# Kernel optimization log

Hardware: AMD Instinct MI355X
Metric: run time of the kernel (lower is better)

Reference implementation:

```python
import jax, jax.numpy as jnp
import numpy as np

N_HEADS = 16
N_KV = 8
HEAD_DIM = 128
HID = 2048
GROUPS = N_HEADS // N_KV
THETA = 10000.0


def _rope_cos_sin(position_ids, dtype):
    # position_ids: [1, S] int
    inv_freq = 1.0 / (THETA ** (jnp.arange(0, HEAD_DIM, 2, dtype=jnp.float32) / HEAD_DIM))
    freqs = position_ids.astype(jnp.float32)[:, :, None] * inv_freq[None, None, :]  # [1,S,hd/2]
    emb = jnp.concatenate([freqs, freqs], axis=-1)  # [1,S,hd]
    return jnp.cos(emb).astype(dtype)[:, None, :, :], jnp.sin(emb).astype(dtype)[:, None, :, :]


def _rotate_half(x):
    x1, x2 = x[..., : HEAD_DIM // 2], x[..., HEAD_DIM // 2 :]
    return jnp.concatenate([-x2, x1], axis=-1)


def setup_inputs() -> dict:
    key = jax.random.key(0)
    ks = jax.random.split(key, 8)
    B, S = 2, 2048
    hidden_states = jax.random.normal(ks[0], (B, S, HID), jnp.float32)
    Wq = jax.random.normal(ks[1], (HID, N_HEADS * HEAD_DIM), jnp.float32) * 0.02
    Wk = jax.random.normal(ks[2], (HID, N_KV * HEAD_DIM), jnp.float32) * 0.02
    Wv = jax.random.normal(ks[3], (HID, N_KV * HEAD_DIM), jnp.float32) * 0.02
    Wo = jax.random.normal(ks[4], (HID, HID), jnp.float32) * 0.02
    gate = jnp.zeros((1, N_HEADS, 1, 1), jnp.float32)
    memory_in = jax.random.normal(ks[5], (B, N_KV, HEAD_DIM, HEAD_DIM), jnp.float32)
    norm_in = jax.random.uniform(ks[6], (B, N_KV, 1, HEAD_DIM), jnp.float32)
    position_ids = jnp.arange(S, dtype=jnp.int32)[None, :]
    return {"hidden_states": hidden_states, "Wq": Wq, "Wk": Wk, "Wv": Wv, "Wo": Wo,
            "gate": gate, "memory_in": memory_in, "norm_in": norm_in,
            "position_ids": position_ids}


def reference(hidden_states, Wq, Wk, Wv, Wo, gate, memory_in, norm_in, position_ids):
    B, S, _ = hidden_states.shape
    # projections -> [B, H, S, hd]
    q = jnp.einsum('bsh,ho->bso', hidden_states, Wq).reshape(B, S, N_HEADS, HEAD_DIM).transpose(0, 2, 1, 3)
    k = jnp.einsum('bsh,ho->bso', hidden_states, Wk).reshape(B, S, N_KV, HEAD_DIM).transpose(0, 2, 1, 3)
    v = jnp.einsum('bsh,ho->bso', hidden_states, Wv).reshape(B, S, N_KV, HEAD_DIM).transpose(0, 2, 1, 3)

    # ---- compressive memory retrieval (pre-RoPE q, as in original) ----
    sigma_q = jax.nn.elu(q) + 1.0  # [B, nH, S, hd]
    mem_tiled = jnp.tile(memory_in, (1, GROUPS, 1, 1))          # torch .repeat tiles
    norm_tiled = jnp.tile(norm_in, (1, GROUPS, 1, 1))            # [B, nH, 1, hd]
    memory_output = jnp.einsum('bhsd,bhde->bhse', sigma_q, mem_tiled)
    norm_bcast = jnp.einsum('bhsd,bhd->bhs', sigma_q, norm_tiled[:, :, 0, :])[..., None]
    memory_output = memory_output / norm_bcast

    # ---- memory update (pre-RoPE k, v) ----
    sigma_k = jax.nn.elu(k) + 1.0  # [B, nKV, S, hd]
    updated_memory = memory_in + jnp.einsum('bhsd,bhse->bhde', sigma_k, v)
    updated_norm = norm_in + jnp.sum(sigma_k, axis=2, keepdims=True)

    # ---- RoPE ----
    cos, sin = _rope_cos_sin(position_ids, q.dtype)
    q = q * cos + _rotate_half(q) * sin
    k = k * cos + _rotate_half(k) * sin

    # ---- repeat_kv (interleave, groups) ----
    k = jnp.repeat(k, GROUPS, axis=1)
    v = jnp.repeat(v, GROUPS, axis=1)

    # ---- causal SDPA ----
    scale = 1.0 / np.sqrt(HEAD_DIM)
    scores = jnp.einsum('bhqd,bhkd->bhqk', q, k) * scale
    causal = jnp.tril(jnp.ones((S, S), dtype=bool))
    scores = jnp.where(causal[None, None], scores, jnp.finfo(scores.dtype).min)
    probs = jax.nn.softmax(scores, axis=-1)
    attn = jnp.einsum('bhqk,bhkd->bhqd', probs, v)

    # ---- gated combination + output projection ----
    g = jax.nn.sigmoid(gate)
    combined = g * memory_output + (1.0 - g) * attn  # [B, nH, S, hd]
    combined = combined.transpose(0, 2, 1, 3).reshape(B, S, HID)
    final_output = jnp.einsum('bsh,ho->bso', combined, Wo)
    return final_output, updated_memory, updated_norm
```

## Files before the change

kernel.cpp:

```cpp
#include <hip/hip_runtime.h>

#define BATCH 2
#define SEQ   2048
#define HID   2048
#define NH    16
#define NKV   8
#define HD    128
#define M_ROWS (BATCH * SEQ)
#define QKV_N  4096

typedef __attribute__((ext_vector_type(8))) __bf16 bf16x8;
typedef __attribute__((ext_vector_type(4))) float  f32x4;

static __device__ __forceinline__ f32x4 mfma16(bf16x8 a, bf16x8 b, f32x4 c) {
    return __builtin_amdgcn_mfma_f32_16x16x32_bf16(a, b, c, 0, 0, 0);
}
static __device__ __forceinline__ float sigma_f(float x) {
    return x > 0.f ? x + 1.f : __expf(x);
}
static __device__ __forceinline__ void gload16(const __bf16* g, __bf16* l) {
    __builtin_amdgcn_global_load_lds(
        (const __attribute__((address_space(1))) void*)g,
        (__attribute__((address_space(3))) void*)l, 16, 0, 0);
}

#define OFF_QKV  0ull
#define OFF_SQ   67108864ull
#define OFF_QR   83886080ull
#define OFF_KR   100663296ull
#define OFF_VT   109051904ull
#define OFF_ND   117440512ull
#define OFF_CB   117702656ull
#define OFF_PART 134479872ull
#define OFF_BND  142868480ull
#define OFF_MAXP 143130624ull
#define OFF_NPART 143134720ull
#define NSPLIT 8

__global__ void f2b_k(const float* __restrict__ src, __bf16* __restrict__ dst)
{
    const size_t i = ((size_t)blockIdx.x * 256 + threadIdx.x) * 8;
    const float4 v0 = *reinterpret_cast<const float4*>(src + i);
    const float4 v1 = *reinterpret_cast<const float4*>(src + i + 4);
    bf16x8 t;
    t[0]=(__bf16)v0.x; t[1]=(__bf16)v0.y; t[2]=(__bf16)v0.z; t[3]=(__bf16)v0.w;
    t[4]=(__bf16)v1.x; t[5]=(__bf16)v1.y; t[6]=(__bf16)v1.z; t[7]=(__bf16)v1.w;
    *reinterpret_cast<bf16x8*>(dst + i) = t;
}

__global__ __launch_bounds__(256) void tr_k(const float* __restrict__ W,
                                            __bf16* __restrict__ Bt, int K, int N)
{
    __shared__ __bf16 T[64][72];
    const int k0 = blockIdx.x * 64, n0 = blockIdx.y * 64;
    const int t = threadIdx.x;
    #pragma unroll
    for (int i = 0; i < 4; ++i) {
        const int idx = t + i * 256;
        const int r = idx >> 4, c4 = (idx & 15) * 4;
        const float4 v = *reinterpret_cast<const float4*>(&W[(size_t)(k0 + r) * N + n0 + c4]);
        T[c4 + 0][r] = (__bf16)v.x; T[c4 + 1][r] = (__bf16)v.y;
        T[c4 + 2][r] = (__bf16)v.z; T[c4 + 3][r] = (__bf16)v.w;
    }
    __syncthreads();
    #pragma unroll
    for (int i = 0; i < 2; ++i) {
        const int idx = t + i * 256;
        const int rr = idx >> 3, cc = (idx & 7) * 8;
        *reinterpret_cast<bf16x8*>(&Bt[(size_t)(n0 + rr) * K + k0 + cc]) =
            *reinterpret_cast<bf16x8*>(&T[rr][cc]);
    }
}

__global__ __launch_bounds__(256) void gemm_bt(const __bf16* __restrict__ A,
                                               const __bf16* __restrict__ Bt,
                                               float* __restrict__ C,
                                               int N, int K)
{
    __shared__ __align__(16) __bf16 As[128 * 32];
    __shared__ __align__(16) __bf16 Bs[128 * 32];

    const int tid = threadIdx.x, wave = tid >> 6, lane = tid & 63;
    const int l15 = lane & 15, l4 = lane >> 4;
    const int m0 = blockIdx.x * 128, n0 = blockIdx.y * 128;
    const int wm = (wave & 1) * 64, wn = (wave >> 1) * 64;

    f32x4 acc[4][4] = {};

    const int srow = wave * 32 + (lane >> 2);
    const int scol = (lane & 3) * 8;
    const __bf16* Ab = A  + (size_t)(m0 + srow) * K + scol;
    const __bf16* Bb = Bt + (size_t)(n0 + srow) * K + scol;
    __bf16* AsB0 = &As[(wave * 32) * 32];
    __bf16* AsB1 = &As[(wave * 32 + 16) * 32];
    __bf16* BsB0 = &Bs[(wave * 32) * 32];
    __bf16* BsB1 = &Bs[(wave * 32 + 16) * 32];

    for (int kb = 0; kb < K; kb += 32) {
        gload16(Ab + kb,            AsB0);
        gload16(Ab + 16 * K + kb,   AsB1);
        gload16(Bb + kb,            BsB0);
        gload16(Bb + 16 * K + kb,   BsB1);
        __syncthreads();

        bf16x8 af[4], bfr[4];
        #pragma unroll
        for (int mt = 0; mt < 4; ++mt)
            af[mt] = *reinterpret_cast<bf16x8*>(&As[(wm + mt * 16 + l15) * 32 + l4 * 8]);
        #pragma unroll
        for (int nt = 0; nt < 4; ++nt)
            bfr[nt] = *reinterpret_cast<bf16x8*>(&Bs[(wn + nt * 16 + l15) * 32 + l4 * 8]);
        #pragma unroll
        for (int mt = 0; mt < 4; ++mt)
            #pragma unroll
            for (int nt = 0; nt < 4; ++nt)
                acc[mt][nt] = mfma16(af[mt], bfr[nt], acc[mt][nt]);
        __syncthreads();
    }

    #pragma unroll
    for (int mt = 0; mt < 4; ++mt)
        #pragma unroll
        for (int nt = 0; nt < 4; ++nt)
            #pragma unroll
            for (int r = 0; r < 4; ++r) {
                const int row = m0 + wm + mt * 16 + l4 * 4 + r;
                const int col = n0 + wn + nt * 16 + l15;
                C[(size_t)row * N + col] = acc[mt][nt][r];
            }
}

__global__ __launch_bounds__(256) void prep_k(const float* __restrict__ qkv,
                                              const float* __restrict__ norm_in,
                                              const int* __restrict__ pos_ids,
                                              __bf16* __restrict__ sq, __bf16* __restrict__ qr,
                                              __bf16* __restrict__ kr, __bf16* __restrict__ vt,
                                              float* __restrict__ nd, float* __restrict__ bnd,
                                              float* __restrict__ maxp)
{
    const int sc = blockIdx.x, kvh = blockIdx.y, b = blockIdx.z;
    const int s0 = sc * 32, t = threadIdx.x;
    const float scale = 0.08838834764831845f;
    const float s2 = scale * scale;
    const float NEG_LN_TH = -0.14391156831212787f;
    __shared__ float krn[32];

    {
        const int row = t >> 2;
        const int head = row >> 5, sl = row & 31;
        const int hq = kvh * 2 + head, nh = hq & 7;
        const int dq = (t & 3) * 16;
        const int pos = pos_ids[s0 + sl];
        const float* qp = qkv + (size_t)(b * SEQ + s0 + sl) * QKV_N + hq * 128;
        const float* np = norm_in + (b * NKV + nh) * 128;

        float x0[16], x1[16];
        #pragma unroll
        for (int i = 0; i < 16; i += 4) {
            *reinterpret_cast<float4*>(&x0[i]) = *reinterpret_cast<const float4*>(qp + dq + i);
            *reinterpret_cast<float4*>(&x1[i]) = *reinterpret_cast<const float4*>(qp + dq + 64 + i);
        }
        float nds = 0.f, qns = 0.f;
        bf16x8 sqv0[2], sqv1[2], qrv0[2], qrv1[2];
        #pragma unroll
        for (int i = 0; i < 16; ++i) {
            const int j = dq + i;
            float c, sn;
            __sincosf((float)pos * __expf((float)j * NEG_LN_TH), &sn, &c);
            qrv0[i >> 3][i & 7] = (__bf16)((x0[i] * c - x1[i] * sn) * scale);
            qrv1[i >> 3][i & 7] = (__bf16)((x1[i] * c + x0[i] * sn) * scale);
            const float sg0 = sigma_f(x0[i]), sg1 = sigma_f(x1[i]);
            sqv0[i >> 3][i & 7] = (__bf16)sg0;
            sqv1[i >> 3][i & 7] = (__bf16)sg1;
            nds += sg0 * np[j] + sg1 * np[j + 64];
            qns += (x0[i] * x0[i] + x1[i] * x1[i]) * s2;
        }
        __bf16* sqp = sq + ((size_t)(b * NH + hq) * SEQ + s0 + sl) * 128;
        __bf16* qrp = qr + ((size_t)(b * NH + hq) * SEQ + s0 + sl) * 128;
        *reinterpret_cast<bf16x8*>(sqp + dq)      = sqv0[0];
        *reinterpret_cast<bf16x8*>(sqp + dq + 8)  = sqv0[1];
        *reinterpret_cast<bf16x8*>(sqp + dq + 64) = sqv1[0];
        *reinterpret_cast<bf16x8*>(sqp + dq + 72) = sqv1[1];
        *reinterpret_cast<bf16x8*>(qrp + dq)      = qrv0[0];
        *reinterpret_cast<bf16x8*>(qrp + dq + 8)  = qrv0[1];
        *reinterpret_cast<bf16x8*>(qrp + dq + 64) = qrv1[0];
        *reinterpret_cast<bf16x8*>(qrp + dq + 72) = qrv1[1];

        nds += __shfl_xor(nds, 1); nds += __shfl_xor(nds, 2);
        qns += __shfl_xor(qns, 1); qns += __shfl_xor(qns, 2);
        if ((t & 3) == 0) {
            nd [(size_t)(b * NH + hq) * SEQ + s0 + sl] = nds;
            bnd[(size_t)(b * NH + hq) * SEQ + s0 + sl] = qns;
        }
    }

    if (t < 128) {
        const int sl = t >> 2;
        const int dq = (t & 3) * 16;
        const int pos = pos_ids[s0 + sl];
        const float* kp = qkv + (size_t)(b * SEQ + s0 + sl) * QKV_N + 2048 + kvh * 128;
        float x0[16], x1[16];
        #pragma unroll
        for (int i = 0; i < 16; i += 4) {
            *reinterpret_cast<float4*>(&x0[i]) = *reinterpret_cast<const float4*>(kp + dq + i);
            *reinterpret_cast<float4*>(&x1[i]) = *reinterpret_cast<const float4*>(kp + dq + 64 + i);
        }
        bf16x8 kv0[2], kv1[2];
        float kns = 0.f;
        #pragma unroll
        for (int i = 0; i < 16; ++i) {
            const int j = dq + i;
            float c, sn;
            __sincosf((float)pos * __expf((float)j * NEG_LN_TH), &sn, &c);
            kv0[i >> 3][i & 7] = (__bf16)(x0[i] * c - x1[i] * sn);
            kv1[i >> 3][i & 7] = (__bf16)(x1[i] * c + x0[i] * sn);
            kns += x0[i] * x0[i] + x1[i] * x1[i];
        }
        __bf16* krp = kr + ((size_t)(b * NKV + kvh) * SEQ + s0 + sl) * 128;
        *reinterpret_cast<bf16x8*>(krp + dq)      = kv0[0];
        *reinterpret_cast<bf16x8*>(krp + dq + 8)  = kv0[1];
        *reinterpret_cast<bf16x8*>(krp + dq + 64) = kv1[0];
        *reinterpret_cast<bf16x8*>(krp + dq + 72) = kv1[1];
        kns += __shfl_xor(kns, 1); kns += __shfl_xor(kns, 2);
        if ((t & 3) == 0) krn[sl] = kns;
    }

    __shared__ float vl[128][33];
    {
        const int sl = t >> 3, dch = (t & 7) * 16;
        const float* vp = qkv + (size_t)(b * SEQ + s0 + sl) * QKV_N + 3072 + kvh * 128 + dch;
        float xv[16];
        #pragma unroll
        for (int i = 0; i < 16; i += 4)
            *reinterpret_cast<float4*>(&xv[i]) = *reinterpret_cast<const float4*>(vp + i);
        #pragma unroll
        for (int i = 0; i < 16; ++i) vl[dch + i][sl] = xv[i];
    }
    __syncthreads();
    if (t == 0) {
        float mx = 0.f;
        #pragma unroll
        for (int i = 0; i < 32; ++i) mx = fmaxf(mx, krn[i]);
        maxp[((b * NKV + kvh) << 6) + sc] = mx;
    }
    {
        const int d = t >> 1, sh = (t & 1) * 16;
        bf16x8 o0, o1;
        #pragma unroll
        for (int j = 0; j < 8; ++j) o0[j] = (__bf16)vl[d][sh + j];
        #pragma unroll
        for (int j = 0; j < 8; ++j) o1[j] = (__bf16)vl[d][sh + 8 + j];
        __bf16* vp = vt + ((size_t)((b * NKV + kvh) * 128 + d)) * SEQ + s0 + sh;
        *reinterpret_cast<bf16x8*>(vp)     = o0;
        *reinterpret_cast<bf16x8*>(vp + 8) = o1;
    }
}

__global__ __launch_bounds__(256) void memout_k(const __bf16* __restrict__ sq,
                                                const float* __restrict__ mem_in,
                                                const float* __restrict__ nd,
                                                const float* __restrict__ gate,
                                                __bf16* __restrict__ cb)
{
    __shared__ __align__(16) __bf16 mt[128][136];
    const int tid = threadIdx.x;
    const int h = blockIdx.y, b = blockIdx.z;
    const int s0 = blockIdx.x * 64;

    const float* mem = mem_in + (size_t)(b * NKV + (h & 7)) * 16384;
    for (int i = tid; i < 16384; i += 256) {
        int dd = i >> 7, e = i & 127;
        mt[e][dd] = (__bf16)mem[i];
    }
    __syncthreads();

    const int wave = tid >> 6, lane = tid & 63, l15 = lane & 15, l4 = lane >> 4;
    f32x4 acc[8] = {};
    const __bf16* sqb = sq + ((size_t)(b * NH + h) * SEQ + s0 + wave * 16 + l15) * 128;
    #pragma unroll
    for (int kb = 0; kb < 4; ++kb) {
        bf16x8 a = *reinterpret_cast<const bf16x8*>(sqb + kb * 32 + l4 * 8);
        #pragma unroll
        for (int nc = 0; nc < 8; ++nc) {
            bf16x8 bb = *reinterpret_cast<bf16x8*>(&mt[nc * 16 + l15][kb * 32 + l4 * 8]);
            acc[nc] = mfma16(a, bb, acc[nc]);
        }
    }
    float g = 1.f / (1.f + __expf(-gate[h]));
    #pragma unroll
    for (int r = 0; r < 4; ++r) {
        int srow = s0 + wave * 16 + l4 * 4 + r;
        float scl = g / nd[(size_t)(b * NH + h) * SEQ + srow];
        __bf16* cbp = cb + (size_t)(b * SEQ + srow) * HID + h * 128;
        #pragma unroll
        for (int nc = 0; nc < 8; ++nc)
            cbp[nc * 16 + l15] = (__bf16)(acc[nc][r] * scl);
    }
}

__global__ __launch_bounds__(256) void memupd_k(const float* __restrict__ qkv,
                                                float* __restrict__ part,
                                                float* __restrict__ npart)
{
    const int sp = blockIdx.x, h = blockIdx.y, b = blockIdx.z;
    const int tid = threadIdx.x;
    const int tx = tid & 15, ty = tid >> 4;
    __shared__ __align__(16) float sk[8][128];
    __shared__ __align__(16) float sv[8][128];
    float acc[8][8] = {};
    float nacc = 0.f;

    const int s0 = sp * (SEQ / NSPLIT);
    for (int so = 0; so < SEQ / NSPLIT; so += 8) {
        for (int i = tid; i < 8 * 128; i += 256) {
            int rr = i >> 7, dd = i & 127;
            const float* rowp = qkv + (size_t)(b * SEQ + s0 + so + rr) * QKV_N;
            sk[rr][dd] = sigma_f(rowp[2048 + h * 128 + dd]);
            sv[rr][dd] = rowp[3072 + h * 128 + dd];
        }
        __syncthreads();
        if (tid < 128) {
            #pragma unroll
            for (int rr = 0; rr < 8; ++rr) nacc += sk[rr][tid];
        }
        #pragma unroll
        for (int rr = 0; rr < 8; ++rr) {
            float4 k0 = *reinterpret_cast<float4*>(&sk[rr][tx * 8]);
            float4 k1 = *reinterpret_cast<float4*>(&sk[rr][tx * 8 + 4]);
            float4 v0 = *reinterpret_cast<float4*>(&sv[rr][ty * 8]);
            float4 v1 = *reinterpret_cast<float4*>(&sv[rr][ty * 8 + 4]);
            float kreg[8] = {k0.x,k0.y,k0.z,k0.w,k1.x,k1.y,k1.z,k1.w};
            float vreg[8] = {v0.x,v0.y,v0.z,v0.w,v1.x,v1.y,v1.z,v1.w};
            #pragma unroll
            for (int i = 0; i < 8; ++i)
                #pragma unroll
                for (int j2 = 0; j2 < 8; ++j2)
                    acc[i][j2] += kreg[i] * vreg[j2];
        }
        __syncthreads();
    }
    float* pb = part + ((size_t)sp * (BATCH * NKV) + b * NKV + h) * 16384;
    #pragma unroll
    for (int i = 0; i < 8; ++i)
        #pragma unroll
        for (int j2 = 0; j2 < 8; ++j2)
            pb[(tx * 8 + i) * 128 + ty * 8 + j2] = acc[i][j2];
    if (tid < 128)
        npart[((size_t)sp * (BATCH * NKV) + b * NKV + h) * 128 + tid] = nacc;
}

__global__ void memred_k(const float* __restrict__ part, const float* __restrict__ mem_in,
                         float* __restrict__ out_mem)
{
    const size_t i = (size_t)blockIdx.x * 256 + threadIdx.x;
    float a = mem_in[i];
    #pragma unroll
    for (int sp = 0; sp < NSPLIT; ++sp) a += part[(size_t)sp * 262144 + i];
    out_mem[i] = a;
}

__global__ void normred_k(const float* __restrict__ npart, const float* __restrict__ norm_in,
                          float* __restrict__ out_norm)
{
    const int bh = blockIdx.x, d = threadIdx.x;
    float a = norm_in[bh * 128 + d];
    #pragma unroll
    for (int sp = 0; sp < NSPLIT; ++sp)
        a += npart[((size_t)sp * (BATCH * NKV) + bh) * 128 + d];
    out_norm[bh * 128 + d] = a;
}

__global__ __launch_bounds__(256, 2) void attn_k(const __bf16* __restrict__ qr,
                                                 const __bf16* __restrict__ kr,
                                                 const __bf16* __restrict__ vt,
                                                 const float* __restrict__ gate,
                                                 const float* __restrict__ bnd,
                                                 const float* __restrict__ maxp,
                                                 __bf16* __restrict__ cb)
{
    __shared__ __align__(16) char smem[81920];
    __bf16* Ks   = (__bf16*)smem;
    __bf16* Vs   = (__bf16*)(smem + 32768);
    __bf16* plds = (__bf16*)(smem + 65536);
    float*  red  = (float*)smem;
    float*  lred = (float*)(smem + 65536);

    const int tid = threadIdx.x, wave = tid >> 6, lane = tid & 63;
    const int l15 = lane & 15, l4 = lane >> 4;

    const int n   = blockIdx.x + 16 * (blockIdx.y + 16 * blockIdx.z);
    const int xcd = n & 7, i64 = n >> 3;
    const int grp = xcd * 2 + (i64 >> 5);
    const int within = i64 & 31;
    const int b   = grp >> 3;
    const int kvh = grp & 7;
    const int h   = kvh * 2 + (within >> 4);
    const int x   = within & 15;

    const __bf16* kbase = kr + (size_t)(b * NKV + kvh) * SEQ * 128;
    const __bf16* vbase = vt + (size_t)(b * NKV + kvh) * 128 * SEQ;
    const float* bbase  = bnd + (size_t)(b * NH + h) * SEQ;

    const float g  = 1.f / (1.f + __expf(-gate[h]));
    const float gi = 1.f - g;
    float kn2 = 0.f;
    const float* mp = maxp + (b * NKV + kvh) * 64;
    #pragma unroll
    for (int i = 0; i < 64; i += 4) {
        const float4 v = *reinterpret_cast<const float4*>(mp + i);
        kn2 = fmaxf(kn2, fmaxf(fmaxf(v.x, v.y), fmaxf(v.z, v.w)));
    }
    const float knmax = sqrtf(kn2);

    bf16x8 ones;
    #pragma unroll
    for (int j = 0; j < 8; ++j) ones[j] = (__bf16)1.0f;

    const int srow = wave * 32 + (lane >> 4);
    __bf16* ksd = Ks + wave * 4096;
    __bf16* vsd = Vs + wave * 4096;

    __bf16* pw = plds + wave * 2048;
    const int ksub = wave >> 1;
    const int wq   = wave & 1;

    #pragma unroll 1
    for (int tile = 0; tile < 2; ++tile) {
        const int q0 = (tile == 0 ? x : 31 - x) * 64;
        const int qw = q0 + wq * 32;
        const int NT = (q0 >> 6) + 1;
        const int NI = (NT + 1) >> 1;

        bf16x8 af[2][4];
        float m_r[2][4];
        #pragma unroll
        for (int m = 0; m < 2; ++m) {
            const __bf16* qb = qr + ((size_t)(b * NH + h) * SEQ + qw + m * 16 + l15) * 128;
            #pragma unroll
            for (int kb = 0; kb < 4; ++kb)
                af[m][kb] = *reinterpret_cast<const bf16x8*>(qb + kb * 32 + l4 * 8);
            #pragma unroll
            for (int r = 0; r < 4; ++r)
                m_r[m][r] = sqrtf(bbase[qw + m * 16 + l4 * 4 + r]) * knmax + 1.0f;
        }

        f32x4 o0[8] = {}, o1[8] = {};
        f32x4 lc0 = {}, lc1 = {};

        #pragma unroll 1
        for (int it = 0; it < NI; ++it) {
            const int kt0 = it * 128;
            #pragma unroll
            for (int j = 0; j < 8; ++j) {
                const int row = srow + j * 4;
                const int ch  = (lane & 15) ^ (row & 7);
                gload16(kbase + (size_t)(kt0 + row) * 128 + ch * 8, ksd + j * 512);
                gload16(vbase + (size_t)row * SEQ + kt0 + ch * 8,   vsd + j * 512);
            }
            __syncthreads();

            const int s = 2 * it + ksub;
            if (s < NT) {
                const int krow0 = ksub * 64;
                f32x4 s0[4] = {}, s1[4] = {};
                #pragma unroll
                for (int kb = 0; kb < 4; ++kb) {
                    #pragma unroll
                    for (int sub = 0; sub < 4; ++sub) {
                        const int krow = krow0 + sub * 16 + l15;
                        bf16x8 bb = *reinterpret_cast<const bf16x8*>(
                            Ks + krow * 128 + (((kb * 4 + l4) ^ (krow & 7)) * 8));
                        s0[sub] = mfma16(af[0][kb], bb, s0[sub]);
                        s1[sub] = mfma16(af[1][kb], bb, s1[sub]);
                    }
                }
                #pragma unroll
                for (int r = 0; r < 4; ++r) {
                    const int q0r = qw + l4 * 4 + r;
                    const int q1r = q0r + 16;
                    const int p0r = l4 * 4 + r, p1r = p0r + 16;
                    #pragma unroll
                    for (int sub = 0; sub < 4; ++sub) {
                        const int key = s * 64 + sub * 16 + l15;
                        float p0 = __expf(s0[sub][r] - m_r[0][r]);
                        float p1 = __expf(s1[sub][r] - m_r[1][r]);
                        p0 = (key <= q0r) ? p0 : 0.f;
                        p1 = (key <= q1r) ? p1 : 0.f;
                        const int cc = (sub * 16 + l15) >> 3, cl = l15 & 7;
                        pw[p0r * 64 + ((cc ^ (p0r & 7)) * 8) + cl] = (__bf16)p0;
                        pw[p1r * 64 + ((cc ^ (p1r & 7)) * 8) + cl] = (__bf16)p1;
                    }
                }
                const int pr1 = 16 + l15;
                bf16x8 a00 = *reinterpret_cast<bf16x8*>(pw + l15 * 64 + ((l4 ^ (l15 & 7)) * 8));
                bf16x8 a01 = *reinterpret_cast<bf16x8*>(pw + l15 * 64 + (((4 + l4) ^ (l15 & 7)) * 8));
                bf16x8 a10 = *reinterpret_cast<bf16x8*>(pw + pr1 * 64 + ((l4 ^ (pr1 & 7)) * 8));
                bf16x8 a11 = *reinterpret_cast<bf16x8*>(pw + pr1 * 64 + (((4 + l4) ^ (pr1 & 7)) * 8));
                lc0 = mfma16(a00, ones, lc0); lc0 = mfma16(a01, ones, lc0);
                lc1 = mfma16(a10, ones, lc1); lc1 = mfma16(a11, ones, lc1);
                #pragma unroll
                for (int nc = 0; nc < 8; ++nc) {
                    const int vrow = nc * 16 + l15;
                    bf16x8 b0 = *reinterpret_cast<bf16x8*>(
                        Vs + vrow * 128 + (((ksub * 8 + l4) ^ (vrow & 7)) * 8));
                    bf16x8 b1 = *reinterpret_cast<bf16x8*>(
                        Vs + vrow * 128 + (((ksub * 8 + 4 + l4) ^ (vrow & 7)) * 8));
                    o0[nc] = mfma16(a00, b0, o0[nc]); o0[nc] = mfma16(a01, b1, o0[nc]);
                    o1[nc] = mfma16(a10, b0, o1[nc]); o1[nc] = mfma16(a11, b1, o1[nc]);
                }
            }
            __syncthreads();
        }

        if (wave >= 2) {
            float* rb = red + (wave - 2) * 4224;
            #pragma unroll
            for (int nc = 0; nc < 8; ++nc)
                #pragma unroll
                for (int r = 0; r < 4; ++r) {
                    rb[(l4 * 4 + r) * 132 + nc * 16 + l15]        = o0[nc][r];
                    rb[(16 + l4 * 4 + r) * 132 + nc * 16 + l15]   = o1[nc][r];
                }
            if (l15 == 0) {
                float* lb = lred + (wave - 2) * 32;
                #pragma unroll
                for (int r = 0; r < 4; ++r) {
                    lb[l4 * 4 + r]      = lc0[r];
                    lb[16 + l4 * 4 + r] = lc1[r];
                }
            }
        }
        __syncthreads();
        if (wave < 2) {
            float* rb = red + wave * 4224;
            const float* lb = lred + wave * 32;
            #pragma unroll
            for (int r = 0; r < 4; ++r) {
                const int qrow = qw + l4 * 4 + r;
                const float i0 = gi / (lc0[r] + lb[l4 * 4 + r]);
                const float i1 = gi / (lc1[r] + lb[16 + l4 * 4 + r]);
                __bf16* c0 = cb + (size_t)(b * SEQ + qrow) * HID + h * 128;
                __bf16* c1 = cb + (size_t)(b * SEQ + qrow + 16) * HID + h * 128;
                #pragma unroll
                for (int nc = 0; nc < 8; ++nc) {
                    const int dd = nc * 16 + l15;
                    const float v0 = o0[nc][r] + rb[(l4 * 4 + r) * 132 + dd];
                    const float v1 = o1[nc][r] + rb[(16 + l4 * 4 + r) * 132 + dd];
                    c0[dd] = (__bf16)((float)c0[dd] + v0 * i0);
                    c1[dd] = (__bf16)((float)c1[dd] + v1 * i1);
                }
            }
        }
        __syncthreads();
    }
}

extern "C" void kernel_launch(void* const* d_in, const int* in_sizes, int n_in,
                              void* d_out, int out_size, void* d_ws, size_t ws_size,
                              hipStream_t stream)
{
    const float* hidden  = (const float*)d_in[0];
    const float* Wq      = (const float*)d_in[1];
    const float* Wk      = (const float*)d_in[2];
    const float* Wv      = (const float*)d_in[3];
    const float* Wo      = (const float*)d_in[4];
    const float* gate    = (const float*)d_in[5];
    const float* mem_in  = (const float*)d_in[6];
    const float* norm_in = (const float*)d_in[7];
    const int*   pos     = (const int*)d_in[8];

    float* out_final = (float*)d_out;
    float* out_mem   = out_final + (size_t)BATCH * SEQ * HID;
    float* out_norm  = out_mem + (size_t)BATCH * NKV * 128 * 128;

    char* ws = (char*)d_ws;
    float*  qkv  = (float*)(ws + OFF_QKV);
    __bf16* sq   = (__bf16*)(ws + OFF_SQ);
    __bf16* qrb  = (__bf16*)(ws + OFF_QR);
    __bf16* krb  = (__bf16*)(ws + OFF_KR);
    __bf16* vtb  = (__bf16*)(ws + OFF_VT);
    float*  nd   = (float*)(ws + OFF_ND);
    __bf16* cb   = (__bf16*)(ws + OFF_CB);
    float*  part = (float*)(ws + OFF_PART);
    float*  bnd  = (float*)(ws + OFF_BND);
    float*  maxp = (float*)(ws + OFF_MAXP);
    float*  npart = (float*)(ws + OFF_NPART);
    __bf16* hb   = (__bf16*)(ws + OFF_SQ);
    __bf16* qkvT = (__bf16*)(ws + OFF_QR);
    __bf16* woT  = (__bf16*)(ws + OFF_PART);

    f2b_k<<<(M_ROWS * HID) / (256 * 8), 256, 0, stream>>>(hidden, hb);
    tr_k<<<dim3(HID / 64, 2048 / 64), 256, 0, stream>>>(Wq, qkvT, HID, 2048);
    tr_k<<<dim3(HID / 64, 1024 / 64), 256, 0, stream>>>(Wk, qkvT + (size_t)2048 * HID, HID, 1024);
    tr_k<<<dim3(HID / 64, 1024 / 64), 256, 0, stream>>>(Wv, qkvT + (size_t)3072 * HID, HID, 1024);

    gemm_bt<<<dim3(M_ROWS / 128, QKV_N / 128), 256, 0, stream>>>(hb, qkvT, qkv, QKV_N, HID);

    prep_k<<<dim3(SEQ / 32, NKV, BATCH), 256, 0, stream>>>(qkv, norm_in, pos, sq, qrb, krb, vtb,
                                                           nd, bnd, maxp);

    memout_k<<<dim3(SEQ / 64, NH, BATCH), 256, 0, stream>>>(sq, mem_in, nd, gate, cb);

    memupd_k<<<dim3(NSPLIT, NKV, BATCH), 256, 0, stream>>>(qkv, part, npart);
    memred_k<<<(BATCH * NKV * 128 * 128) / 256, 256, 0, stream>>>(part, mem_in, out_mem);
    normred_k<<<BATCH * NKV, 128, 0, stream>>>(npart, norm_in, out_norm);

    tr_k<<<dim3(HID / 64, HID / 64), 256, 0, stream>>>(Wo, woT, HID, HID);

    attn_k<<<dim3(16, NH, BATCH), 256, 0, stream>>>(qrb, krb, vtb, gate, bnd, maxp, cb);

    gemm_bt<<<dim3(M_ROWS / 128, HID / 128), 256, 0, stream>>>(cb, woT, out_final, HID, HID);
}
```

Before: 475.0 us.

## Replace GEMM with 256x256-tile 8-wave kernel using double-buffered async LDS pipeline

```diff
diff --git a/kernel.cpp b/kernel.cpp
--- a/kernel.cpp
+++ b/kernel.cpp
@@ -72,62 +72,139 @@
     }
 }
 
-__global__ __launch_bounds__(256) void gemm_bt(const __bf16* __restrict__ A,
-                                               const __bf16* __restrict__ Bt,
-                                               float* __restrict__ C,
-                                               int N, int K)
-{
-    __shared__ __align__(16) __bf16 As[128 * 32];
-    __shared__ __align__(16) __bf16 Bs[128 * 32];
-
+__global__ __launch_bounds__(512, 2) void gemm8_k(const __bf16* __restrict__ A,
+                                                  const __bf16* __restrict__ Bt,
+                                                  float* __restrict__ C,
+                                                  int N, int K)
+{
+    __shared__ __align__(16) __bf16 smem[65536];
     const int tid = threadIdx.x, wave = tid >> 6, lane = tid & 63;
     const int l15 = lane & 15, l4 = lane >> 4;
-    const int m0 = blockIdx.x * 128, n0 = blockIdx.y * 128;
-    const int wm = (wave & 1) * 64, wn = (wave >> 1) * 64;
-
-    f32x4 acc[4][4] = {};
-
-    const int srow = wave * 32 + (lane >> 2);
-    const int scol = (lane & 3) * 8;
-    const __bf16* Ab = A  + (size_t)(m0 + srow) * K + scol;
-    const __bf16* Bb = Bt + (size_t)(n0 + srow) * K + scol;
-    __bf16* AsB0 = &As[(wave * 32) * 32];
-    __bf16* AsB1 = &As[(wave * 32 + 16) * 32];
-    __bf16* BsB0 = &Bs[(wave * 32) * 32];
-    __bf16* BsB1 = &Bs[(wave * 32 + 16) * 32];
-
-    for (int kb = 0; kb < K; kb += 32) {
-        gload16(Ab + kb,            AsB0);
-        gload16(Ab + 16 * K + kb,   AsB1);
-        gload16(Bb + kb,            BsB0);
-        gload16(Bb + 16 * K + kb,   BsB1);
-        __syncthreads();
-
-        bf16x8 af[4], bfr[4];
-        #pragma unroll
-        for (int mt = 0; mt < 4; ++mt)
-            af[mt] = *reinterpret_cast<bf16x8*>(&As[(wm + mt * 16 + l15) * 32 + l4 * 8]);
-        #pragma unroll
-        for (int nt = 0; nt < 4; ++nt)
-            bfr[nt] = *reinterpret_cast<bf16x8*>(&Bs[(wn + nt * 16 + l15) * 32 + l4 * 8]);
-        #pragma unroll
-        for (int mt = 0; mt < 4; ++mt)
-            #pragma unroll
-            for (int nt = 0; nt < 4; ++nt)
-                acc[mt][nt] = mfma16(af[mt], bfr[nt], acc[mt][nt]);
-        __syncthreads();
-    }
-
-    #pragma unroll
-    for (int mt = 0; mt < 4; ++mt)
-        #pragma unroll
-        for (int nt = 0; nt < 4; ++nt)
-            #pragma unroll
-            for (int r = 0; r < 4; ++r) {
-                const int row = m0 + wm + mt * 16 + l4 * 4 + r;
-                const int col = n0 + wn + nt * 16 + l15;
-                C[(size_t)row * N + col] = acc[mt][nt][r];
-            }
+    const int wr = wave >> 2, wc = wave & 3;
+
+    const int nwg = gridDim.x;
+    const int swz = (blockIdx.x & 7) * (nwg >> 3) + (blockIdx.x >> 3);
+    const int NBN = N >> 8;
+    const int bm = swz / NBN, bn = swz - bm * NBN;
+    const int m0 = bm << 8, n0 = bn << 8;
+
+    const int NKT = K >> 6;
+
+    const int srow   = tid >> 2;
+    const int schunk = (tid & 3) ^ ((tid >> 3) & 3);
+    const int sdst   = wave * 512;
+
+    const int achunk = l4 ^ ((l15 >> 1) & 3);
+    const int aoff = (wr * 128 + l15) * 32 + achunk * 8;
+    const int boff = (wc * 64  + l15) * 32 + achunk * 8;
+
+    f32x4 acc[2][4][4] = {};
+    bf16x8 af[4], bfr[4];
+
+#define STAGE_SLAB(gb, r0, koff, slabptr) do {                                   \
+        const __bf16* _g = (gb) + (size_t)((r0) + srow) * K + (koff) + schunk * 8; \
+        gload16(_g,                    (slabptr) + sdst);                        \
+        gload16(_g + (size_t)128 * K,  (slabptr) + sdst + 4096);                 \
+    } while (0)
+
+    STAGE_SLAB(A,  m0, 0,  smem);
+    STAGE_SLAB(Bt, n0, 0,  smem + 16384);
+    STAGE_SLAB(A,  m0, 32, smem + 8192);
+    STAGE_SLAB(Bt, n0, 32, smem + 24576);
+    STAGE_SLAB(A,  m0, 64, smem + 32768);
+    STAGE_SLAB(Bt, n0, 64, smem + 32768 + 16384);
+    asm volatile("s_waitcnt vmcnt(4)" ::: "memory");
+    __builtin_amdgcn_s_barrier();
+
+    #pragma unroll 1
+    for (int T = 0; T < NKT; ++T) {
+        __bf16* bufc = smem + (T & 1) * 32768;
+        __bf16* bufn = smem + ((T & 1) ^ 1) * 32768;
+        const int kt1 = (T + 1) * 64, kt2 = (T + 2) * 64;
+
+        {
+            const __bf16* As = bufc;
+            const __bf16* Bs = bufc + 16384;
+            #pragma unroll
+            for (int f = 0; f < 4; ++f)  af[f]  = *reinterpret_cast<const bf16x8*>(As + aoff + f * 512);
+            #pragma unroll
+            for (int nf = 0; nf < 4; ++nf) bfr[nf] = *reinterpret_cast<const bf16x8*>(Bs + boff + nf * 512);
+            if (T + 1 < NKT) STAGE_SLAB(A, m0, kt1 + 32, bufn + 8192);
+            __builtin_amdgcn_s_barrier();
+            __builtin_amdgcn_s_setprio(1);
+            #pragma unroll
+            for (int f = 0; f < 4; ++f)
+                #pragma unroll
+                for (int nf = 0; nf < 4; ++nf)
+                    acc[0][f][nf] = mfma16(af[f], bfr[nf], acc[0][f][nf]);
+            __builtin_amdgcn_s_setprio(0);
+            __builtin_amdgcn_s_barrier();
+        }
+        {
+            const __bf16* As = bufc;
+            #pragma unroll
+            for (int f = 0; f < 4; ++f)  af[f] = *reinterpret_cast<const bf16x8*>(As + aoff + 2048 + f * 512);
+            if (T + 1 < NKT) STAGE_SLAB(Bt, n0, kt1 + 32, bufn + 24576);
+            __builtin_amdgcn_s_barrier();
+            __builtin_amdgcn_s_setprio(1);
+            #pragma unroll
+            for (int f = 0; f < 4; ++f)
+                #pragma unroll
+                for (int nf = 0; nf < 4; ++nf)
+                    acc[1][f][nf] = mfma16(af[f], bfr[nf], acc[1][f][nf]);
+            __builtin_amdgcn_s_setprio(0);
+            __builtin_amdgcn_s_barrier();
+        }
+        {
+            const __bf16* As = bufc + 8192;
+            const __bf16* Bs = bufc + 24576;
+            #pragma unroll
+            for (int f = 0; f < 4; ++f)  af[f]  = *reinterpret_cast<const bf16x8*>(As + aoff + f * 512);
+            #pragma unroll
+            for (int nf = 0; nf < 4; ++nf) bfr[nf] = *reinterpret_cast<const bf16x8*>(Bs + boff + nf * 512);
+            if (T + 2 < NKT) STAGE_SLAB(A, m0, kt2, bufc);
+            __builtin_amdgcn_s_barrier();
+            __builtin_amdgcn_s_setprio(1);
+            #pragma unroll
+            for (int f = 0; f < 4; ++f)
+                #pragma unroll
+                for (int nf = 0; nf < 4; ++nf)
+                    acc[0][f][nf] = mfma16(af[f], bfr[nf], acc[0][f][nf]);
+            __builtin_amdgcn_s_setprio(0);
+            __builtin_amdgcn_s_barrier();
+        }
+        {
+            const __bf16* As = bufc + 8192;
+            #pragma unroll
+            for (int f = 0; f < 4; ++f)  af[f] = *reinterpret_cast<const bf16x8*>(As + aoff + 2048 + f * 512);
+            if (T + 2 < NKT) STAGE_SLAB(Bt, n0, kt2, bufc + 16384);
+            __builtin_amdgcn_s_barrier();
+            __builtin_amdgcn_s_setprio(1);
+            #pragma unroll
+            for (int f = 0; f < 4; ++f)
+                #pragma unroll
+                for (int nf = 0; nf < 4; ++nf)
+                    acc[1][f][nf] = mfma16(af[f], bfr[nf], acc[1][f][nf]);
+            __builtin_amdgcn_s_setprio(0);
+            if (T < NKT - 2) asm volatile("s_waitcnt vmcnt(4)" ::: "memory");
+            else             asm volatile("s_waitcnt vmcnt(0)" ::: "memory");
+            __builtin_amdgcn_s_barrier();
+        }
+    }
+#undef STAGE_SLAB
+
+    #pragma unroll
+    for (int mh = 0; mh < 2; ++mh)
+        #pragma unroll
+        for (int f = 0; f < 4; ++f)
+            #pragma unroll
+            for (int nf = 0; nf < 4; ++nf)
+                #pragma unroll
+                for (int r = 0; r < 4; ++r) {
+                    const int row = m0 + wr * 128 + mh * 64 + f * 16 + l4 * 4 + r;
+                    const int col = n0 + wc * 64 + nf * 16 + l15;
+                    C[(size_t)row * N + col] = acc[mh][f][nf][r];
+                }
 }
 
 __global__ __launch_bounds__(256) void prep_k(const float* __restrict__ qkv,
@@ -594,7 +671,7 @@
     tr_k<<<dim3(HID / 64, 1024 / 64), 256, 0, stream>>>(Wk, qkvT + (size_t)2048 * HID, HID, 1024);
     tr_k<<<dim3(HID / 64, 1024 / 64), 256, 0, stream>>>(Wv, qkvT + (size_t)3072 * HID, HID, 1024);
 
-    gemm_bt<<<dim3(M_ROWS / 128, QKV_N / 128), 256, 0, stream>>>(hb, qkvT, qkv, QKV_N, HID);
+    gemm8_k<<<(M_ROWS / 256) * (QKV_N / 256), 512, 0, stream>>>(hb, qkvT, qkv, QKV_N, HID);
 
     prep_k<<<dim3(SEQ / 32, NKV, BATCH), 256, 0, stream>>>(qkv, norm_in, pos, sq, qrb, krb, vtb,
                                                            nd, bnd, maxp);
@@ -609,5 +686,5 @@
 
     attn_k<<<dim3(16, NH, BATCH), 256, 0, stream>>>(qrb, krb, vtb, gate, bnd, maxp, cb);
 
-    gemm_bt<<<dim3(M_ROWS / 128, HID / 128), 256, 0, stream>>>(cb, woT, out_final, HID, HID);
-}
+    gemm8_k<<<(M_ROWS / 256) * (HID / 256), 512, 0, stream>>>(cb, woT, out_final, HID, HID);
+}
```

Measured after the change: 462.7 us. 1.03x faster.
